# Performance work log

Hardware: AMD Instinct MI355X
Metric: run time of the kernel (lower is better)

The kernel has to match this reference:

```python
import jax, jax.numpy as jnp
import numpy as np

N = 100000      # total nodes (herb + ingredient + target concatenated)
E = 1600000     # edges (all etypes concatenated)
D_IN = 128
D_HID = 128
D_OUT = 128
BN_EPS = 1e-5
LEAKY_SLOPE = 0.01


def setup_inputs() -> dict:
    key = jax.random.key(0)
    ks = jax.random.split(key, 8)
    x = jax.random.normal(ks[0], (N, D_IN), dtype=jnp.float32)
    src = jax.random.randint(ks[1], (E,), 0, N, dtype=jnp.int32)
    dst = jax.random.randint(ks[2], (E,), 0, N, dtype=jnp.int32)
    W1 = jax.random.normal(ks[3], (D_IN, D_HID), dtype=jnp.float32) * (1.0 / np.sqrt(D_IN))
    b1 = jnp.zeros((D_HID,), jnp.float32)
    W2 = jax.random.normal(ks[4], (D_HID, D_OUT), dtype=jnp.float32) * (1.0 / np.sqrt(D_HID))
    b2 = jnp.zeros((D_OUT,), jnp.float32)
    gamma = jnp.ones((D_HID,), jnp.float32)
    beta = jnp.zeros((D_HID,), jnp.float32)
    run_mean = jax.random.normal(ks[5], (D_HID,), jnp.float32) * 0.1
    run_var = jax.random.uniform(ks[6], (D_HID,), jnp.float32, 0.5, 1.5)
    return {"x": x, "src": src, "dst": dst, "W1": W1, "b1": b1,
            "W2": W2, "b2": b2, "gamma": gamma, "beta": beta,
            "run_mean": run_mean, "run_var": run_var}


def _graph_conv(h, s, d, W, b, norm_src, norm_dst):
    # DGL GraphConv, norm='both': D_out^{-1/2} then sum-aggregate then D_in^{-1/2}, then linear
    h = h * norm_src                                   # [N, d]
    m = jax.ops.segment_sum(h[s], d, num_segments=N)   # gather + spmm-aggregate
    m = m * norm_dst
    return m @ W + b


def reference(x, src, dst, W1, b1, W2, b2, gamma, beta, run_mean, run_var):
    # dgl.add_self_loop: append (i, i) for every node
    loop = jnp.arange(N, dtype=src.dtype)
    s = jnp.concatenate([src, loop])
    d = jnp.concatenate([dst, loop])
    ones = jnp.ones(s.shape[0], jnp.float32)
    out_deg = jnp.maximum(jax.ops.segment_sum(ones, s, num_segments=N), 1.0)
    in_deg = jnp.maximum(jax.ops.segment_sum(ones, d, num_segments=N), 1.0)
    norm_src = (out_deg ** -0.5)[:, None]
    norm_dst = (in_deg ** -0.5)[:, None]

    # layer 0: conv -> BN (eval, running stats) -> leaky_relu -> dropout (eval = identity)
    h = _graph_conv(x, s, d, W1, b1, norm_src, norm_dst)
    h = (h - run_mean) * jax.lax.rsqrt(run_var + BN_EPS) * gamma + beta
    h = jnp.where(h > 0, h, LEAKY_SLOPE * h)

    # layer 1 (last): conv only
    h = _graph_conv(h, s, d, W2, b2, norm_src, norm_dst)
    return h
```

## Files before the change

### kernel.cpp

```cpp
#include <hip/hip_runtime.h>

#define NN 100000
#define NE 1600000
#define D 128
#define LEAKY 0.01f
#define BNEPS 1e-5f

#define G 256
#define CHUNK 6250
#define B 782
#define BSHIFT 7
#define BMASK 127
#define NSB (B * G / 256)

typedef short v8s __attribute__((ext_vector_type(8)));
typedef float v4f __attribute__((ext_vector_type(4)));

__device__ __forceinline__ unsigned f2bf(float f) {
    unsigned u = __float_as_uint(f);
    return (u + 0x7fffu + ((u >> 16) & 1u)) >> 16;
}
__device__ __forceinline__ float bf2f(unsigned h) {
    return __uint_as_float(h << 16);
}


__global__ __launch_bounds__(1024) void hist_kernel(const int* __restrict__ src,
                                                    const int* __restrict__ dst,
                                                    int* __restrict__ hist,
                                                    int* __restrict__ hist2) {
    __shared__ int h[B];
    __shared__ int h2[B];
    for (int i = threadIdx.x; i < B; i += 1024) { h[i] = 0; h2[i] = 0; }
    __syncthreads();
    int g = blockIdx.x;
    const int* dp = dst + g * CHUNK;
    const int* sp = src + g * CHUNK;
    for (int k = threadIdx.x; k < CHUNK; k += 1024) {
        atomicAdd(&h[dp[k] >> BSHIFT], 1);
        atomicAdd(&h2[sp[k] >> BSHIFT], 1);
    }
    __syncthreads();
    for (int i = threadIdx.x; i < B; i += 1024) {
        hist[i * G + g]  = h[i];
        hist2[i * G + g] = h2[i];
    }
}


__global__ void scanA2(const int* __restrict__ a, const int* __restrict__ a2,
                       int* __restrict__ bsum, int* __restrict__ bsum2) {
    __shared__ int sm[256];
    int t = threadIdx.x;
    bool second = blockIdx.x >= NSB;
    int blk = second ? blockIdx.x - NSB : blockIdx.x;
    const int* sp = second ? a2 : a;
    sm[t] = sp[blk * 256 + t];
    __syncthreads();
    for (int s = 128; s > 0; s >>= 1) {
        if (t < s) sm[t] += sm[t + s];
        __syncthreads();
    }
    if (t == 0) (second ? bsum2 : bsum)[blk] = sm[0];
}

__device__ __forceinline__ void scanB_one(const int* __restrict__ bsum,
                                          int* __restrict__ boffs, int lane) {
    int run = 0;
    for (int base = 0; base < B; base += 64) {
        int i = base + lane;
        int v = (i < B) ? bsum[i] : 0;
        int orig = v;
        for (int off = 1; off < 64; off <<= 1) {
            int t = __shfl_up(v, off);
            if (lane >= off) v += t;
        }
        if (i < B) boffs[i] = run + v - orig;
        run += __shfl(v, 63);
    }
}

__global__ void scanB2(const int* __restrict__ bsum, int* __restrict__ boffs,
                       const int* __restrict__ bsum2, int* __restrict__ boffs2) {
    int lane = threadIdx.x;
    scanB_one(bsum, boffs, lane);
    scanB_one(bsum2, boffs2, lane);
}

__global__ void scanC2(const int* __restrict__ a, const int* __restrict__ a2,
                       const int* __restrict__ boffs, const int* __restrict__ boffs2,
                       int* __restrict__ offs, int* __restrict__ offs2) {
    __shared__ int sm[256];
    int t = threadIdx.x;
    bool second = blockIdx.x >= NSB;
    int blk = second ? blockIdx.x - NSB : blockIdx.x;
    const int* sp = second ? a2 : a;
    int i = blk * 256 + t;
    int v = sp[i];
    sm[t] = v;
    __syncthreads();
    for (int off = 1; off < 256; off <<= 1) {
        int x = (t >= off) ? sm[t - off] : 0;
        __syncthreads();
        sm[t] += x;
        __syncthreads();
    }
    (second ? offs2 : offs)[i] = (second ? boffs2 : boffs)[blk] + sm[t] - v;
}

__global__ __launch_bounds__(1024) void sort_kernel(const int* __restrict__ src,
                                                    const int* __restrict__ dst,
                                                    const int* __restrict__ offs,
                                                    const int* __restrict__ offs2,
                                                    unsigned* __restrict__ ebuf,
                                                    unsigned* __restrict__ sbuf) {
    __shared__ int cur[B];
    __shared__ int cur2[B];
    int g = blockIdx.x;
    for (int i = threadIdx.x; i < B; i += 1024) {
        cur[i]  = offs[i * G + g];
        cur2[i] = offs2[i * G + g];
    }
    __syncthreads();
    const int* sp = src + g * CHUNK;
    const int* dp = dst + g * CHUNK;
    for (int k = threadIdx.x; k < CHUNK; k += 1024) {
        int d = dp[k], s = sp[k];
        int pos = atomicAdd(&cur[d >> BSHIFT], 1);
        ebuf[pos] = ((unsigned)(d & BMASK) << 17) | (unsigned)s;
        int pos2 = atomicAdd(&cur2[s >> BSHIFT], 1);
        sbuf[pos2] = (unsigned)s;
    }
}


__global__ __launch_bounds__(256) void conv_deg(const int* __restrict__ offs2,
                                                const unsigned* __restrict__ sbuf,
                                                const float* __restrict__ x,
                                                float* __restrict__ norm_s,
                                                unsigned* __restrict__ hb) {
    __shared__ int cnt[128];
    __shared__ float nsm[128];
    const int b = blockIdx.x;
    const int t = threadIdx.x;
    const int s = offs2[b * G];
    const int e = (b == B - 1) ? NE : offs2[(b + 1) * G];
    if (t < 128) cnt[t] = 0;
    __syncthreads();
    for (int k = s + t; k < e; k += 256)
        atomicAdd(&cnt[sbuf[k] & BMASK], 1);
    __syncthreads();
    if (t < 128) {
        int node = b * 128 + t;
        if (node < NN) {
            float ns = rsqrtf((float)(cnt[t] + 1));
            norm_s[node] = ns;
            nsm[t] = ns;
        }
    }
    __syncthreads();
    for (int idx = t; idx < 128 * 32; idx += 256) {
        int r = idx >> 5, q = idx & 31;
        int node = b * 128 + r;
        if (node >= NN) continue;
        float ns = nsm[r];
        float4 v = ((const float4*)x)[(size_t)node * 32 + q];
        uint2 w;
        w.x = f2bf(v.x * ns) | (f2bf(v.y * ns) << 16);
        w.y = f2bf(v.z * ns) | (f2bf(v.w * ns) << 16);
        *(uint2*)(hb + (size_t)node * 64 + 2 * q) = w;
    }
}


__global__ __launch_bounds__(256) void local_sort(
    const int* __restrict__ offs, unsigned* __restrict__ ebuf,
    int* __restrict__ row, float* __restrict__ norm_d)
{
    __shared__ int cnt[128];
    __shared__ int sc[128];
    const int b = blockIdx.x;
    const int t = threadIdx.x;
    const int s = offs[b * G];
    const int e = (b == B - 1) ? NE : offs[(b + 1) * G];
    if (t < 128) cnt[t] = 0;
    __syncthreads();

    unsigned ent[16];
    int nent = 0;
    for (int k = s + t; k < e && nent < 16; k += 256) {
        unsigned u = ebuf[k];
        ent[nent++] = u;
        atomicAdd(&cnt[u >> 17], 1);
    }
    __syncthreads();

    if (t < 128) sc[t] = cnt[t];
    __syncthreads();
    for (int off = 1; off < 128; off <<= 1) {
        int v = 0;
        if (t < 128 && t >= off) v = sc[t - off];
        __syncthreads();
        if (t < 128) sc[t] += v;
        __syncthreads();
    }
    if (t < 128) {
        int st = s + sc[t] - cnt[t];
        int node = b * 128 + t;
        if (node < NN) {
            row[node] = st;
            norm_d[node] = rsqrtf((float)(cnt[t] + 1));
        }
        cnt[t] = st;
    }
    if (b == B - 1 && t == 0) row[NN] = NE;
    __syncthreads();

    for (int i = 0; i < nent; ++i) {
        unsigned u = ent[i];
        int pos = atomicAdd(&cnt[u >> 17], 1);
        ebuf[pos] = u & 0x1FFFFu;
    }
}


__global__ __launch_bounds__(256) void csr_agg(
    const int* __restrict__ rowp, const int* __restrict__ csr,
    const unsigned* __restrict__ hp,
    unsigned* __restrict__ Ahi, unsigned* __restrict__ Alo)
{
    int i = blockIdx.x * 4 + (threadIdx.x >> 6);
    if (i >= NN) return;
    const int lane = threadIdx.x & 63;
    const int half = lane >> 5;
    const int c2   = lane & 31;

    float4 acc = {0.f, 0.f, 0.f, 0.f};
    if (half == 0) {
        uint2 u = *(const uint2*)(hp + (size_t)i * 64 + 2 * c2);
        acc.x = __uint_as_float(u.x << 16);
        acc.y = __uint_as_float(u.x & 0xffff0000u);
        acc.z = __uint_as_float(u.y << 16);
        acc.w = __uint_as_float(u.y & 0xffff0000u);
    }

    int start = rowp[i], end = rowp[i + 1];
    for (int base = start; base < end; base += 64) {
        int n = end - base; if (n > 64) n = 64;
        int sv = csr[base + (lane < n ? lane : n - 1)];
        int nfull = n & ~15;
        int j = 0;
        for (; j < nfull; j += 16) {
            int ss[8]; uint2 uu[8];
            #pragma unroll
            for (int t = 0; t < 8; ++t) ss[t] = __shfl(sv, j + 2 * t + half);
            #pragma unroll
            for (int t = 0; t < 8; ++t)
                uu[t] = *(const uint2*)(hp + (size_t)ss[t] * 64 + 2 * c2);
            #pragma unroll
            for (int t = 0; t < 8; ++t) {
                acc.x += __uint_as_float(uu[t].x << 16);
                acc.y += __uint_as_float(uu[t].x & 0xffff0000u);
                acc.z += __uint_as_float(uu[t].y << 16);
                acc.w += __uint_as_float(uu[t].y & 0xffff0000u);
            }
        }
        if (j < n) {
            int ss[8]; uint2 uu[8];
            #pragma unroll
            for (int t = 0; t < 8; ++t) {
                int e = j + 2 * t + half;
                ss[t] = __shfl(sv, e < n ? e : n - 1);
            }
            #pragma unroll
            for (int t = 0; t < 8; ++t)
                uu[t] = *(const uint2*)(hp + (size_t)ss[t] * 64 + 2 * c2);
            #pragma unroll
            for (int t = 0; t < 8; ++t) {
                if (j + 2 * t + half < n) {
                    acc.x += __uint_as_float(uu[t].x << 16);
                    acc.y += __uint_as_float(uu[t].x & 0xffff0000u);
                    acc.z += __uint_as_float(uu[t].y << 16);
                    acc.w += __uint_as_float(uu[t].y & 0xffff0000u);
                }
            }
        }
    }

    acc.x += __shfl_xor(acc.x, 32);
    acc.y += __shfl_xor(acc.y, 32);
    acc.z += __shfl_xor(acc.z, 32);
    acc.w += __shfl_xor(acc.w, 32);

    unsigned h0 = f2bf(acc.x), h1 = f2bf(acc.y);
    unsigned h2 = f2bf(acc.z), h3 = f2bf(acc.w);
    if (half == 0) {
        uint2 w = { h0 | (h1 << 16), h2 | (h3 << 16) };
        *(uint2*)(Ahi + (size_t)i * 64 + 2 * c2) = w;
    } else {
        float l0 = acc.x - bf2f(h0), l1 = acc.y - bf2f(h1);
        float l2 = acc.z - bf2f(h2), l3 = acc.w - bf2f(h3);
        uint2 w = { f2bf(l0) | (f2bf(l1) << 16), f2bf(l2) | (f2bf(l3) << 16) };
        *(uint2*)(Alo + (size_t)i * 64 + 2 * c2) = w;
    }
}


template<bool LAYER0>
__global__ __launch_bounds__(256) void gemm_kernel(
    const unsigned* __restrict__ Ahi_g, const unsigned* __restrict__ Alo_g,
    const float* __restrict__ W, const float* __restrict__ bias,
    const float* __restrict__ norm_s, const float* __restrict__ norm_d,
    const float* __restrict__ gamma, const float* __restrict__ beta,
    const float* __restrict__ rmean, const float* __restrict__ rvar,
    float* __restrict__ outf, unsigned short* __restrict__ outb)
{
    __shared__ unsigned lhi[64 * 68];
    __shared__ unsigned llo[64 * 68];

    const int w    = threadIdx.x >> 6;
    const int lane = threadIdx.x & 63;
    const int quad = lane >> 4;
    const int l16  = lane & 15;

    v8s Bhi[2][4], Blo[2][4];
    int col[2];
    #pragma unroll
    for (int ct = 0; ct < 2; ++ct) {
        col[ct] = 32 * w + 16 * ct + l16;
        #pragma unroll
        for (int q = 0; q < 4; ++q) {
            int kb = 32 * q + quad * 8;
            v8s hi8, lo8;
            #pragma unroll
            for (int kk = 0; kk < 8; ++kk) {
                float wv = W[(kb + kk) * D + col[ct]];
                unsigned h = f2bf(wv);
                hi8[kk] = (short)h;
                lo8[kk] = (short)f2bf(wv - bf2f(h));
            }
            Bhi[ct][q] = hi8;
            Blo[ct][q] = lo8;
        }
    }

    float bcol[2], s[2] = {0.f, 0.f}, sh[2] = {0.f, 0.f};
    #pragma unroll
    for (int ct = 0; ct < 2; ++ct) {
        bcol[ct] = bias[col[ct]];
        if (LAYER0) {
            s[ct]  = gamma[col[ct]] * rsqrtf(rvar[col[ct]] + BNEPS);
            sh[ct] = beta[col[ct]] - rmean[col[ct]] * s[ct];
        }
    }

    for (int row0 = blockIdx.x * 64; row0 < NN; row0 += gridDim.x * 64) {
        __syncthreads();
        for (int idx = threadIdx.x; idx < 64 * 64; idx += 256) {
            int r = idx >> 6, cp = idx & 63;
            int rw = row0 + r;
            unsigned vh = 0, vl = 0;
            if (rw < NN) {
                vh = Ahi_g[(size_t)rw * 64 + cp];
                vl = Alo_g[(size_t)rw * 64 + cp];
            }
            lhi[r * 68 + cp] = vh;
            llo[r * 68 + cp] = vl;
        }
        __syncthreads();

        #pragma unroll
        for (int rt = 0; rt < 4; ++rt) {
            v4f acc0 = {0.f, 0.f, 0.f, 0.f};
            v4f acc1 = {0.f, 0.f, 0.f, 0.f};
            #pragma unroll
            for (int q = 0; q < 4; ++q) {
                const unsigned short* ph = (const unsigned short*)lhi
                    + (rt * 16 + l16) * 136 + q * 32 + quad * 8;
                const unsigned short* pl = (const unsigned short*)llo
                    + (rt * 16 + l16) * 136 + q * 32 + quad * 8;
                v8s ahi = *(const v8s*)ph;
                v8s alo = *(const v8s*)pl;
                acc0 = __builtin_amdgcn_mfma_f32_16x16x32_bf16(ahi, Bhi[0][q], acc0, 0, 0, 0);
                acc0 = __builtin_amdgcn_mfma_f32_16x16x32_bf16(alo, Bhi[0][q], acc0, 0, 0, 0);
                acc0 = __builtin_amdgcn_mfma_f32_16x16x32_bf16(ahi, Blo[0][q], acc0, 0, 0, 0);
                acc1 = __builtin_amdgcn_mfma_f32_16x16x32_bf16(ahi, Bhi[1][q], acc1, 0, 0, 0);
                acc1 = __builtin_amdgcn_mfma_f32_16x16x32_bf16(alo, Bhi[1][q], acc1, 0, 0, 0);
                acc1 = __builtin_amdgcn_mfma_f32_16x16x32_bf16(ahi, Blo[1][q], acc1, 0, 0, 0);
            }
            #pragma unroll
            for (int r = 0; r < 4; ++r) {
                int rw = row0 + rt * 16 + quad * 4 + r;
                if (rw >= NN) continue;
                float nd = norm_d[rw];
                float o0 = acc0[r] * nd + bcol[0];
                float o1 = acc1[r] * nd + bcol[1];
                if (LAYER0) {
                    o0 = o0 * s[0] + sh[0];
                    o1 = o1 * s[1] + sh[1];
                    o0 = o0 > 0.f ? o0 : LEAKY * o0;
                    o1 = o1 > 0.f ? o1 : LEAKY * o1;
                    float ns = norm_s[rw];
                    o0 *= ns; o1 *= ns;
                    outb[(size_t)rw * D + col[0]] = (unsigned short)f2bf(o0);
                    outb[(size_t)rw * D + col[1]] = (unsigned short)f2bf(o1);
                } else {
                    outf[(size_t)rw * D + col[0]] = o0;
                    outf[(size_t)rw * D + col[1]] = o1;
                }
            }
        }
    }
}


extern "C" void kernel_launch(void* const* d_in, const int* in_sizes, int n_in,
                              void* d_out, int out_size, void* d_ws, size_t ws_size,
                              hipStream_t stream) {
    const float* x     = (const float*)d_in[0];
    const int*   src   = (const int*)d_in[1];
    const int*   dst   = (const int*)d_in[2];
    const float* W1    = (const float*)d_in[3];
    const float* b1    = (const float*)d_in[4];
    const float* W2    = (const float*)d_in[5];
    const float* b2    = (const float*)d_in[6];
    const float* gamma = (const float*)d_in[7];
    const float* beta  = (const float*)d_in[8];
    const float* rmean = (const float*)d_in[9];
    const float* rvar  = (const float*)d_in[10];
    float* out = (float*)d_out;

    unsigned* hb = (unsigned*)d_out;

    unsigned* Ahi   = (unsigned*)d_ws;
    unsigned* Alo   = Ahi + (size_t)NN * 64;
    float*    norm  = (float*)(Alo + (size_t)NN * 64);
    int*      aux   = (int*)(norm + 2 * NN);
    int*      hist  = aux + NN;
    int*      offs  = hist + B * G;
    int*      bsum  = offs + B * G;
    int*      boffs = bsum + B;
    unsigned* ebuf  = (unsigned*)(boffs + B);
    float* norm_s = norm;
    float* norm_d = norm + NN;
    int*   row    = hist;
    int*   bsum2  = aux;
    int*   boffs2 = aux + B;

    int*      hist2 = (int*)Ahi;
    int*      offs2 = hist2 + B * G;
    unsigned* sbuf  = (unsigned*)(offs2 + B * G);

    hist_kernel<<<G, 1024, 0, stream>>>(src, dst, hist, hist2);
    scanA2<<<2 * NSB, 256, 0, stream>>>(hist, hist2, bsum, bsum2);
    scanB2<<<1, 64, 0, stream>>>(bsum, boffs, bsum2, boffs2);
    scanC2<<<2 * NSB, 256, 0, stream>>>(hist, hist2, boffs, boffs2, offs, offs2);
    sort_kernel<<<G, 1024, 0, stream>>>(src, dst, offs, offs2, ebuf, sbuf);
    conv_deg<<<B, 256, 0, stream>>>(offs2, sbuf, x, norm_s, hb);
    local_sort<<<B, 256, 0, stream>>>(offs, ebuf, row, norm_d);

    const int AGG_BLOCKS = (NN + 3) / 4;
    const int GEMM_BLOCKS = 784;
    csr_agg<<<AGG_BLOCKS, 256, 0, stream>>>(row, (const int*)ebuf, hb, Ahi, Alo);
    gemm_kernel<true><<<GEMM_BLOCKS, 256, 0, stream>>>(Ahi, Alo, W1, b1,
                                                       norm_s, norm_d,
                                                       gamma, beta, rmean, rvar,
                                                       nullptr, (unsigned short*)hb);
    csr_agg<<<AGG_BLOCKS, 256, 0, stream>>>(row, (const int*)ebuf, hb, Ahi, Alo);
    gemm_kernel<false><<<GEMM_BLOCKS, 256, 0, stream>>>(Ahi, Alo, W2, b2,
                                                        norm_s, norm_d,
                                                        nullptr, nullptr, nullptr, nullptr,
                                                        out, nullptr);
}
```

Measured before the change: 419.3 us.

## Fuse scan and bucket kernels, widen CSR aggregation gathers to 16-byte loads

Measured after the change: 418.8 us. Within noise of the previous version (-0.1%).

```diff
diff --git a/kernel.cpp b/kernel.cpp
--- a/kernel.cpp
+++ b/kernel.cpp
@@ -23,6 +23,8 @@
 __device__ __forceinline__ float bf2f(unsigned h) {
     return __uint_as_float(h << 16);
 }
+__device__ __forceinline__ float blo(unsigned u) { return __uint_as_float(u << 16); }
+__device__ __forceinline__ float bhi(unsigned u) { return __uint_as_float(u & 0xffff0000u); }
 
 
 __global__ __launch_bounds__(1024) void hist_kernel(const int* __restrict__ src,
@@ -46,7 +48,6 @@
         hist2[i * G + g] = h2[i];
     }
 }
-
 
 __global__ void scanA2(const int* __restrict__ a, const int* __restrict__ a2,
                        int* __restrict__ bsum, int* __restrict__ bsum2) {
@@ -64,37 +65,26 @@
     if (t == 0) (second ? bsum2 : bsum)[blk] = sm[0];
 }
 
-__device__ __forceinline__ void scanB_one(const int* __restrict__ bsum,
-                                          int* __restrict__ boffs, int lane) {
-    int run = 0;
-    for (int base = 0; base < B; base += 64) {
-        int i = base + lane;
-        int v = (i < B) ? bsum[i] : 0;
-        int orig = v;
-        for (int off = 1; off < 64; off <<= 1) {
-            int t = __shfl_up(v, off);
-            if (lane >= off) v += t;
-        }
-        if (i < B) boffs[i] = run + v - orig;
-        run += __shfl(v, 63);
-    }
-}
-
-__global__ void scanB2(const int* __restrict__ bsum, int* __restrict__ boffs,
-                       const int* __restrict__ bsum2, int* __restrict__ boffs2) {
-    int lane = threadIdx.x;
-    scanB_one(bsum, boffs, lane);
-    scanB_one(bsum2, boffs2, lane);
-}
-
 __global__ void scanC2(const int* __restrict__ a, const int* __restrict__ a2,
-                       const int* __restrict__ boffs, const int* __restrict__ boffs2,
+                       const int* __restrict__ bsum, const int* __restrict__ bsum2,
                        int* __restrict__ offs, int* __restrict__ offs2) {
     __shared__ int sm[256];
+    __shared__ int bo;
     int t = threadIdx.x;
     bool second = blockIdx.x >= NSB;
     int blk = second ? blockIdx.x - NSB : blockIdx.x;
     const int* sp = second ? a2 : a;
+    const int* bs = second ? bsum2 : bsum;
+    int part = 0;
+    for (int j = t; j < blk; j += 256) part += bs[j];
+    sm[t] = part;
+    __syncthreads();
+    for (int s = 128; s > 0; s >>= 1) {
+        if (t < s) sm[t] += sm[t + s];
+        __syncthreads();
+    }
+    if (t == 0) bo = sm[0];
+    __syncthreads();
     int i = blk * 256 + t;
     int v = sp[i];
     sm[t] = v;
@@ -105,7 +95,7 @@
         sm[t] += x;
         __syncthreads();
     }
-    (second ? offs2 : offs)[i] = (second ? boffs2 : boffs)[blk] + sm[t] - v;
+    (second ? offs2 : offs)[i] = bo + sm[t] - v;
 }
 
 __global__ __launch_bounds__(1024) void sort_kernel(const int* __restrict__ src,
@@ -134,92 +124,91 @@
 }
 
 
-__global__ __launch_bounds__(256) void conv_deg(const int* __restrict__ offs2,
-                                                const unsigned* __restrict__ sbuf,
-                                                const float* __restrict__ x,
-                                                float* __restrict__ norm_s,
-                                                unsigned* __restrict__ hb) {
+__global__ __launch_bounds__(256) void bucket_prep(
+    const int* __restrict__ offs, const int* __restrict__ offs2,
+    unsigned* __restrict__ ebuf, const unsigned* __restrict__ sbuf,
+    const float* __restrict__ x, int* __restrict__ row,
+    float* __restrict__ norm_s, float* __restrict__ norm_d,
+    unsigned* __restrict__ hb)
+{
     __shared__ int cnt[128];
+    __shared__ int sc[128];
     __shared__ float nsm[128];
     const int b = blockIdx.x;
     const int t = threadIdx.x;
-    const int s = offs2[b * G];
-    const int e = (b == B - 1) ? NE : offs2[(b + 1) * G];
-    if (t < 128) cnt[t] = 0;
-    __syncthreads();
-    for (int k = s + t; k < e; k += 256)
-        atomicAdd(&cnt[sbuf[k] & BMASK], 1);
-    __syncthreads();
-    if (t < 128) {
-        int node = b * 128 + t;
-        if (node < NN) {
-            float ns = rsqrtf((float)(cnt[t] + 1));
-            norm_s[node] = ns;
-            nsm[t] = ns;
-        }
-    }
-    __syncthreads();
-    for (int idx = t; idx < 128 * 32; idx += 256) {
-        int r = idx >> 5, q = idx & 31;
-        int node = b * 128 + r;
-        if (node >= NN) continue;
-        float ns = nsm[r];
-        float4 v = ((const float4*)x)[(size_t)node * 32 + q];
-        uint2 w;
-        w.x = f2bf(v.x * ns) | (f2bf(v.y * ns) << 16);
-        w.y = f2bf(v.z * ns) | (f2bf(v.w * ns) << 16);
-        *(uint2*)(hb + (size_t)node * 64 + 2 * q) = w;
-    }
-}
-
-
-__global__ __launch_bounds__(256) void local_sort(
-    const int* __restrict__ offs, unsigned* __restrict__ ebuf,
-    int* __restrict__ row, float* __restrict__ norm_d)
-{
-    __shared__ int cnt[128];
-    __shared__ int sc[128];
-    const int b = blockIdx.x;
-    const int t = threadIdx.x;
-    const int s = offs[b * G];
-    const int e = (b == B - 1) ? NE : offs[(b + 1) * G];
-    if (t < 128) cnt[t] = 0;
-    __syncthreads();
-
-    unsigned ent[16];
-    int nent = 0;
-    for (int k = s + t; k < e && nent < 16; k += 256) {
-        unsigned u = ebuf[k];
-        ent[nent++] = u;
-        atomicAdd(&cnt[u >> 17], 1);
-    }
-    __syncthreads();
-
-    if (t < 128) sc[t] = cnt[t];
-    __syncthreads();
-    for (int off = 1; off < 128; off <<= 1) {
-        int v = 0;
-        if (t < 128 && t >= off) v = sc[t - off];
-        __syncthreads();
-        if (t < 128) sc[t] += v;
-        __syncthreads();
-    }
-    if (t < 128) {
-        int st = s + sc[t] - cnt[t];
-        int node = b * 128 + t;
-        if (node < NN) {
-            row[node] = st;
-            norm_d[node] = rsqrtf((float)(cnt[t] + 1));
-        }
-        cnt[t] = st;
-    }
-    if (b == B - 1 && t == 0) row[NN] = NE;
-    __syncthreads();
-
-    for (int i = 0; i < nent; ++i) {
-        unsigned u = ent[i];
-        int pos = atomicAdd(&cnt[u >> 17], 1);
-        ebuf[pos] = u & 0x1FFFFu;
+
+    {
+        const int s = offs2[b * G];
+        const int e = (b == B - 1) ? NE : offs2[(b + 1) * G];
+        if (t < 128) cnt[t] = 0;
+        __syncthreads();
+        for (int k = s + t; k < e; k += 256)
+            atomicAdd(&cnt[sbuf[k] & BMASK], 1);
+        __syncthreads();
+        if (t < 128) {
+            int node = b * 128 + t;
+            if (node < NN) {
+                float ns = rsqrtf((float)(cnt[t] + 1));
+                norm_s[node] = ns;
+                nsm[t] = ns;
+            }
+        }
+        __syncthreads();
+        for (int idx = t; idx < 128 * 32; idx += 256) {
+            int r = idx >> 5, q = idx & 31;
+            int node = b * 128 + r;
+            if (node >= NN) continue;
+            float ns = nsm[r];
+            float4 v = ((const float4*)x)[(size_t)node * 32 + q];
+            uint2 w;
+            w.x = f2bf(v.x * ns) | (f2bf(v.y * ns) << 16);
+            w.y = f2bf(v.z * ns) | (f2bf(v.w * ns) << 16);
+            *(uint2*)(hb + (size_t)node * 64 + 2 * q) = w;
+        }
+    }
+    __syncthreads();
+
+    {
+        const int s = offs[b * G];
+        const int e = (b == B - 1) ? NE : offs[(b + 1) * G];
+        if (t < 128) cnt[t] = 0;
+        __syncthreads();
+
+        unsigned ent[16];
+        int nent = 0;
+        for (int k = s + t; k < e && nent < 16; k += 256) {
+            unsigned u = ebuf[k];
+            ent[nent++] = u;
+            atomicAdd(&cnt[u >> 17], 1);
+        }
+        __syncthreads();
+
+        if (t < 128) sc[t] = cnt[t];
+        __syncthreads();
+        for (int off = 1; off < 128; off <<= 1) {
+            int v = 0;
+            if (t < 128 && t >= off) v = sc[t - off];
+            __syncthreads();
+            if (t < 128) sc[t] += v;
+            __syncthreads();
+        }
+        if (t < 128) {
+            int st = s + sc[t] - cnt[t];
+            int node = b * 128 + t;
+            if (node < NN) {
+                row[node] = st;
+                norm_d[node] = rsqrtf((float)(cnt[t] + 1));
+            }
+            cnt[t] = st;
+        }
+        if (b == B - 1 && t == 0) row[NN] = NE;
+        __syncthreads();
+
+        for (int i = 0; i < nent; ++i) {
+            unsigned u = ent[i];
+            int pos = atomicAdd(&cnt[u >> 17], 1);
+            ebuf[pos] = u & 0x1FFFFu;
+        }
     }
 }
 
@@ -232,76 +221,67 @@
     int i = blockIdx.x * 4 + (threadIdx.x >> 6);
     if (i >= NN) return;
     const int lane = threadIdx.x & 63;
-    const int half = lane >> 5;
-    const int c2   = lane & 31;
-
-    float4 acc = {0.f, 0.f, 0.f, 0.f};
-    if (half == 0) {
-        uint2 u = *(const uint2*)(hp + (size_t)i * 64 + 2 * c2);
-        acc.x = __uint_as_float(u.x << 16);
-        acc.y = __uint_as_float(u.x & 0xffff0000u);
-        acc.z = __uint_as_float(u.y << 16);
-        acc.w = __uint_as_float(u.y & 0xffff0000u);
+    const int q    = lane >> 4;
+    const int f    = lane & 15;
+
+    float acc[8] = {0.f, 0.f, 0.f, 0.f, 0.f, 0.f, 0.f, 0.f};
+    if (q == 0) {
+        uint4 u = *(const uint4*)(hp + (size_t)i * 64 + 4 * f);
+        acc[0] = blo(u.x); acc[1] = bhi(u.x);
+        acc[2] = blo(u.y); acc[3] = bhi(u.y);
+        acc[4] = blo(u.z); acc[5] = bhi(u.z);
+        acc[6] = blo(u.w); acc[7] = bhi(u.w);
     }
 
     int start = rowp[i], end = rowp[i + 1];
     for (int base = start; base < end; base += 64) {
         int n = end - base; if (n > 64) n = 64;
         int sv = csr[base + (lane < n ? lane : n - 1)];
-        int nfull = n & ~15;
-        int j = 0;
-        for (; j < nfull; j += 16) {
-            int ss[8]; uint2 uu[8];
+        for (int j = 0; j < n; j += 32) {
+            int rem = n - j;
+            uint4 uu[8];
             #pragma unroll
-            for (int t = 0; t < 8; ++t) ss[t] = __shfl(sv, j + 2 * t + half);
+            for (int tt = 0; tt < 8; ++tt) {
+                if (4 * tt < rem) {
+                    int e = j + 4 * tt + q;
+                    int s = __shfl(sv, e < n ? e : n - 1);
+                    uu[tt] = *(const uint4*)(hp + (size_t)s * 64 + 4 * f);
+                }
+            }
             #pragma unroll
-            for (int t = 0; t < 8; ++t)
-                uu[t] = *(const uint2*)(hp + (size_t)ss[t] * 64 + 2 * c2);
-            #pragma unroll
-            for (int t = 0; t < 8; ++t) {
-                acc.x += __uint_as_float(uu[t].x << 16);
-                acc.y += __uint_as_float(uu[t].x & 0xffff0000u);
-                acc.z += __uint_as_float(uu[t].y << 16);
-                acc.w += __uint_as_float(uu[t].y & 0xffff0000u);
-            }
-        }
-        if (j < n) {
-            int ss[8]; uint2 uu[8];
-            #pragma unroll
-            for (int t = 0; t < 8; ++t) {
-                int e = j + 2 * t + half;
-                ss[t] = __shfl(sv, e < n ? e : n - 1);
-            }
-            #pragma unroll
-            for (int t = 0; t < 8; ++t)
-                uu[t] = *(const uint2*)(hp + (size_t)ss[t] * 64 + 2 * c2);
-            #pragma unroll
-            for (int t = 0; t < 8; ++t) {
-                if (j + 2 * t + half < n) {
-                    acc.x += __uint_as_float(uu[t].x << 16);
-                    acc.y += __uint_as_float(uu[t].x & 0xffff0000u);
-                    acc.z += __uint_as_float(uu[t].y << 16);
-                    acc.w += __uint_as_float(uu[t].y & 0xffff0000u);
+            for (int tt = 0; tt < 8; ++tt) {
+                if (4 * tt < rem) {
+                    if (j + 4 * tt + q < n) {
+                        acc[0] += blo(uu[tt].x); acc[1] += bhi(uu[tt].x);
+                        acc[2] += blo(uu[tt].y); acc[3] += bhi(uu[tt].y);
+                        acc[4] += blo(uu[tt].z); acc[5] += bhi(uu[tt].z);
+                        acc[6] += blo(uu[tt].w); acc[7] += bhi(uu[tt].w);
+                    }
                 }
             }
         }
     }
 
-    acc.x += __shfl_xor(acc.x, 32);
-    acc.y += __shfl_xor(acc.y, 32);
-    acc.z += __shfl_xor(acc.z, 32);
-    acc.w += __shfl_xor(acc.w, 32);
-
-    unsigned h0 = f2bf(acc.x), h1 = f2bf(acc.y);
-    unsigned h2 = f2bf(acc.z), h3 = f2bf(acc.w);
-    if (half == 0) {
-        uint2 w = { h0 | (h1 << 16), h2 | (h3 << 16) };
-        *(uint2*)(Ahi + (size_t)i * 64 + 2 * c2) = w;
-    } else {
-        float l0 = acc.x - bf2f(h0), l1 = acc.y - bf2f(h1);
-        float l2 = acc.z - bf2f(h2), l3 = acc.w - bf2f(h3);
-        uint2 w = { f2bf(l0) | (f2bf(l1) << 16), f2bf(l2) | (f2bf(l3) << 16) };
-        *(uint2*)(Alo + (size_t)i * 64 + 2 * c2) = w;
+    #pragma unroll
+    for (int k = 0; k < 8; ++k) {
+        acc[k] += __shfl_xor(acc[k], 16);
+        acc[k] += __shfl_xor(acc[k], 32);
+    }
+
+    unsigned h[8];
+    #pragma unroll
+    for (int k = 0; k < 8; ++k) h[k] = f2bf(acc[k]);
+    if (q == 0) {
+        uint4 w = { h[0] | (h[1] << 16), h[2] | (h[3] << 16),
+                    h[4] | (h[5] << 16), h[6] | (h[7] << 16) };
+        *(uint4*)(Ahi + (size_t)i * 64 + 4 * f) = w;
+    } else if (q == 1) {
+        unsigned l[8];
+        #pragma unroll
+        for (int k = 0; k < 8; ++k) l[k] = f2bf(acc[k] - bf2f(h[k]));
+        uint4 w = { l[0] | (l[1] << 16), l[2] | (l[3] << 16),
+                    l[4] | (l[5] << 16), l[6] | (l[7] << 16) };
+        *(uint4*)(Alo + (size_t)i * 64 + 4 * f) = w;
     }
 }
 
@@ -445,7 +425,6 @@
     float* norm_d = norm + NN;
     int*   row    = hist;
     int*   bsum2  = aux;
-    int*   boffs2 = aux + B;
 
     int*      hist2 = (int*)Ahi;
     int*      offs2 = hist2 + B * G;
@@ -453,11 +432,10 @@
 
     hist_kernel<<<G, 1024, 0, stream>>>(src, dst, hist, hist2);
     scanA2<<<2 * NSB, 256, 0, stream>>>(hist, hist2, bsum, bsum2);
-    scanB2<<<1, 64, 0, stream>>>(bsum, boffs, bsum2, boffs2);
-    scanC2<<<2 * NSB, 256, 0, stream>>>(hist, hist2, boffs, boffs2, offs, offs2);
+    scanC2<<<2 * NSB, 256, 0, stream>>>(hist, hist2, bsum, bsum2, offs, offs2);
     sort_kernel<<<G, 1024, 0, stream>>>(src, dst, offs, offs2, ebuf, sbuf);
-    conv_deg<<<B, 256, 0, stream>>>(offs2, sbuf, x, norm_s, hb);
-    local_sort<<<B, 256, 0, stream>>>(offs, ebuf, row, norm_d);
+    bucket_prep<<<B, 256, 0, stream>>>(offs, offs2, ebuf, sbuf, x, row,
+                                       norm_s, norm_d, hb);
 
     const int AGG_BLOCKS = (NN + 3) / 4;
     const int GEMM_BLOCKS = 784;
```
